# Kernel tuning notes

Hardware: AMD Instinct MI355X
Metric: run time of the kernel (lower is better)

The kernel has to match this reference:

```python
import jax, jax.numpy as jnp
import numpy as np

NEG_BIG = -1e12
ALPHA = 0.2  # LeakyReLU negative slope

def setup_inputs() -> dict:
    key = jax.random.key(0)
    k1, k2, k3, k4, k5 = jax.random.split(key, 5)
    N, F_in, F_out = 8192, 256, 128
    inp = jax.random.normal(k1, (N, F_in), dtype=jnp.float32)
    adj = jax.random.randint(k2, (N, N), 0, 2, dtype=jnp.int32)
    W = jax.random.normal(k3, (F_in, F_out), dtype=jnp.float32) * 0.05
    W_2 = jax.random.normal(k4, (F_in, F_out), dtype=jnp.float32) * 0.05
    W_3 = jax.random.normal(k5, (F_in, F_out), dtype=jnp.float32) * 0.05
    return {"inp": inp, "adj": adj, "W": W, "W_2": W_2, "W_3": W_3}

def reference(inp, adj, W, W_2, W_3):
    # h = inp @ W, h_2 = inp @ W_2  -> scores e = LeakyReLU(h @ h_2^T)  [N, N]
    h = inp @ W
    h_2 = inp @ W_2
    e = jax.nn.leaky_relu(h @ h_2.T, negative_slope=ALPHA)
    # adjacency mask, row softmax (dropout disabled: eval mode)
    attention = jax.nn.softmax(jnp.where(adj > 0, e, NEG_BIG), axis=1)
    h_3 = inp @ W_3
    h_prime = attention @ h_3
    return jax.nn.elu(h_prime)  # concat=True path
```

## Files before the change

kernel.cpp:

```cpp
#include <hip/hip_runtime.h>
#include <hip/hip_fp16.h>

#define N    8192
#define FIN  256
#define FOUT 128
#define BN   64

typedef _Float16 half8 __attribute__((ext_vector_type(8)));
typedef _Float16 half4v __attribute__((ext_vector_type(4)));
typedef float floatx4 __attribute__((ext_vector_type(4)));

__device__ __forceinline__ float exp2_fast(float x) { return __builtin_amdgcn_exp2f(x); }

__device__ __forceinline__ void gload_lds16(const void* g, void* l) {
    __builtin_amdgcn_global_load_lds(
        (const __attribute__((address_space(1))) void*)g,
        (__attribute__((address_space(3))) void*)l, 16, 0, 0);
}

__global__ __launch_bounds__(256)
void wprep_kernel(const float* __restrict__ W0,
                  const float* __restrict__ W1,
                  const float* __restrict__ W2,
                  _Float16* __restrict__ Wf)
{
    int idx  = blockIdx.x * 256 + threadIdx.x;
    int lane = idx & 63;
    int frag = idx >> 6;
    int w    = frag >> 6;
    int f    = frag & 63;
    int nt   = f >> 3, kc = f & 7;
    int quad = lane >> 4, lo16 = lane & 15;
    const float* Wp = w == 0 ? W0 : (w == 1 ? W1 : W2);
    half8 v;
#pragma unroll
    for (int jj = 0; jj < 8; jj++)
        v[jj] = (_Float16)Wp[(size_t)(kc * 32 + quad * 8 + jj) * FOUT + nt * 16 + lo16];
    *(half8*)&Wf[(size_t)idx * 8] = v;
}

__global__ __launch_bounds__(256, 2)
void gemm3_kernel(const float* __restrict__ inp,
                  const _Float16* __restrict__ Wf,
                  _Float16* __restrict__ H,
                  _Float16* __restrict__ H2,
                  _Float16* __restrict__ H3T)
{
    const int which = blockIdx.z;
    const int c0    = blockIdx.y * 64;
    const _Float16* Wfw = Wf + (size_t)which * 64 * 64 * 8;
    const int r0 = blockIdx.x * 64;
    const int tid  = threadIdx.x;
    const int wave = tid >> 6;
    const int lane = tid & 63;
    const int lo16 = lane & 15;
    const int quad = lane >> 4;
    const int r = r0 + wave * 16 + lo16;

    half8 a[8];
#pragma unroll
    for (int kc = 0; kc < 8; kc++) {
        const float* p = &inp[(size_t)r * FIN + kc * 32 + quad * 8];
        float4 v0 = *(const float4*)p;
        float4 v1 = *(const float4*)(p + 4);
        a[kc][0] = (_Float16)v0.x; a[kc][1] = (_Float16)v0.y;
        a[kc][2] = (_Float16)v0.z; a[kc][3] = (_Float16)v0.w;
        a[kc][4] = (_Float16)v1.x; a[kc][5] = (_Float16)v1.y;
        a[kc][6] = (_Float16)v1.z; a[kc][7] = (_Float16)v1.w;
    }

    floatx4 acc[4];
#pragma unroll
    for (int i = 0; i < 4; i++) acc[i] = (floatx4){0.f, 0.f, 0.f, 0.f};

#pragma unroll
    for (int kc = 0; kc < 8; kc++)
#pragma unroll
        for (int nt = 0; nt < 4; nt++) {
            int ntg = (c0 >> 4) + nt;
            half8 b = *(const half8*)&Wfw[(((size_t)ntg * 8 + kc) * 64 + lane) * 8];
            acc[nt] = __builtin_amdgcn_mfma_f32_16x16x32_f16(a[kc], b, acc[nt], 0, 0, 0);
        }

    const int arow = wave * 16 + quad * 4;
    if (which < 2) {
        _Float16* outp = which == 0 ? H : H2;
        const float scale = which == 0 ? 1.44269504f : 1.0f;
#pragma unroll
        for (int nt = 0; nt < 4; nt++)
#pragma unroll
            for (int rr = 0; rr < 4; rr++)
                outp[(size_t)(r0 + arow + rr) * FOUT + c0 + nt * 16 + lo16] =
                    (_Float16)(acc[nt][rr] * scale);
    } else {
#pragma unroll
        for (int nt = 0; nt < 4; nt++) {
            half4v v;
#pragma unroll
            for (int rr = 0; rr < 4; rr++) v[rr] = (_Float16)acc[nt][rr];
            *(half4v*)&H3T[(size_t)(c0 + nt * 16 + lo16) * N + r0 + arow] = v;
        }
    }
}

__global__ __launch_bounds__(256)
void repackKV_kernel(const _Float16* __restrict__ H2,
                     const _Float16* __restrict__ H3T,
                     _Float16* __restrict__ Kf,
                     _Float16* __restrict__ Vf)
{
    if (blockIdx.x < 512) {
        int idx  = blockIdx.x * 256 + threadIdx.x;
        int lane = idx & 63;
        int frag = idx >> 6;
        int jb = frag >> 4, f = frag & 15;
        int c = f >> 3, ntj = (f >> 2) & 1, kc = f & 3;
        int quad = lane >> 4, lo16 = lane & 15;
        int srcrow = jb * 64 + c * 32 + (lo16 >> 2) * 8 + ntj * 4 + (lo16 & 3);
        half8 v = *(const half8*)&H2[(size_t)srcrow * FOUT + kc * 32 + quad * 8];
        *(half8*)&Kf[(size_t)idx * 8] = v;
    } else {
        int idx  = (blockIdx.x - 512) * 256 + threadIdx.x;
        int lane = idx & 63;
        int frag = idx >> 6;
        int jb = frag >> 4, f = frag & 15, nt = f >> 1, kc = f & 1;
        int quad = lane >> 4, lo16 = lane & 15;
        half8 v = *(const half8*)&H3T[(size_t)(nt * 16 + lo16) * N + jb * 64 + kc * 32 + quad * 8];
        *(half8*)&Vf[(size_t)idx * 8] = v;
    }
}

template<int JS>
__global__ __launch_bounds__(256, 2)
void attn_kernel(const _Float16* __restrict__ Hq,
                 const _Float16* __restrict__ Kf,
                 const _Float16* __restrict__ Vf,
                 const int* __restrict__ adj,
                 float* __restrict__ OpartT,
                 float* __restrict__ mpart,
                 float* __restrict__ lpart)
{
    __shared__ __align__(16) _Float16 KV[2][16384];

    const int tid  = threadIdx.x;
    const int wave = tid >> 6;
    const int lane = tid & 63;
    const int lo16 = lane & 15;
    const int quad = lane >> 4;
    const int bid  = blockIdx.x;
    const int js   = bid & (JS - 1);
    const int ib   = bid / JS;
    const int iw   = ib * 128 + wave * 32;
    const int jbeg = js * (N / JS);
    const int NIT  = (N / JS) / BN;
    const int jb0  = jbeg >> 6;

    half8 q[2][4];
#pragma unroll
    for (int isub = 0; isub < 2; isub++)
#pragma unroll
        for (int kc = 0; kc < 4; kc++)
            q[isub][kc] = *(const half8*)&Hq[(size_t)(iw + isub * 16 + lo16) * FOUT + kc * 32 + quad * 8];

    floatx4 O[8][2];
#pragma unroll
    for (int nt = 0; nt < 8; nt++)
#pragma unroll
        for (int s = 0; s < 2; s++) O[nt][s] = (floatx4){0.f, 0.f, 0.f, 0.f};
    float m_s[2] = {-1e12f, -1e12f}, l_s[2] = {0.f, 0.f};

    const int* abase0 = adj + (size_t)(iw + lo16) * N + jbeg + quad * 8;
    const int* abase1 = abase0 + (size_t)16 * N;

    int4 avA[8], avB[8];

    auto LOADAV = [&](int4 (&av)[8], int it) {
        const int* b0 = abase0 + it * BN;
        const int* b1 = abase1 + it * BN;
        av[0] = *(const int4*)(b0 + 0);
        av[1] = *(const int4*)(b0 + 4);
        av[2] = *(const int4*)(b0 + 32);
        av[3] = *(const int4*)(b0 + 36);
        av[4] = *(const int4*)(b1 + 0);
        av[5] = *(const int4*)(b1 + 4);
        av[6] = *(const int4*)(b1 + 32);
        av[7] = *(const int4*)(b1 + 36);
    };

    auto STAGE = [&](int nxt, int jbn) {
        const _Float16* gk = Kf + (size_t)jbn * 8192;
        const _Float16* gv = Vf + (size_t)jbn * 8192;
#pragma unroll
        for (int r = 0; r < 4; r++) {
            int goff = (r * 256 + tid) * 8;
            int loff = (r * 256 + wave * 64) * 8;
            gload_lds16(gk + goff, &KV[nxt][loff]);
            gload_lds16(gv + goff, &KV[nxt][8192 + loff]);
        }
    };

    STAGE(0, jb0);
    LOADAV(avA, 0);
    __syncthreads();

    auto ITER = [&](int it, int4 (&avc)[8], int4 (&avn)[8], int cur) {
        if (it + 1 < NIT) {
            STAGE(cur ^ 1, jb0 + it + 1);
            LOADAV(avn, it + 1);
        }

        const _Float16* kb = &KV[cur][0];
        const _Float16* vb = &KV[cur][8192];

        floatx4 S[2][2][2];
#pragma unroll
        for (int c = 0; c < 2; c++)
#pragma unroll
            for (int ntj = 0; ntj < 2; ntj++) {
                S[c][ntj][0] = (floatx4){0.f, 0.f, 0.f, 0.f};
                S[c][ntj][1] = (floatx4){0.f, 0.f, 0.f, 0.f};
#pragma unroll
                for (int kc = 0; kc < 4; kc++) {
                    half8 kf = *(const half8*)&kb[(((c * 2 + ntj) * 4 + kc) * 64 + lane) * 8];
                    S[c][ntj][0] = __builtin_amdgcn_mfma_f32_16x16x32_f16(kf, q[0][kc], S[c][ntj][0], 0, 0, 0);
                    S[c][ntj][1] = __builtin_amdgcn_mfma_f32_16x16x32_f16(kf, q[1][kc], S[c][ntj][1], 0, 0, 0);
                }
            }

        half8 pb[2][2];
#pragma unroll
        for (int s = 0; s < 2; s++) {
            float mx = -1e12f;
#pragma unroll
            for (int c = 0; c < 2; c++)
#pragma unroll
                for (int ntj = 0; ntj < 2; ntj++)
#pragma unroll
                    for (int r = 0; r < 4; r++) {
                        float e = S[c][ntj][s][r];
                        e = fmaxf(e, 0.2f * e);
                        S[c][ntj][s][r] = e;
                        mx = fmaxf(mx, e);
                    }
            mx = fmaxf(mx, __shfl_xor(mx, 16));
            mx = fmaxf(mx, __shfl_xor(mx, 32));
            if (__any(mx > m_s[s] + 5.75f)) {
                float mn = fmaxf(m_s[s], mx);
                float al = exp2_fast(m_s[s] - mn);
                m_s[s] = mn;
                l_s[s] *= al;
#pragma unroll
                for (int nt = 0; nt < 8; nt++)
#pragma unroll
                    for (int r = 0; r < 4; r++)
                        O[nt][s][r] *= al;
            }

            float sum = 0.f;
#pragma unroll
            for (int c = 0; c < 2; c++)
#pragma unroll
                for (int ntj = 0; ntj < 2; ntj++) {
                    int4 av = avc[s * 4 + c * 2 + ntj];
#pragma unroll
                    for (int r = 0; r < 4; r++) {
                        float e = S[c][ntj][s][r] - m_s[s];
                        int a = (r == 0) ? av.x : (r == 1) ? av.y : (r == 2) ? av.z : av.w;
                        float p = (a != 0) ? exp2_fast(e) : 0.f;
                        sum += p;
                        pb[s][c][ntj * 4 + r] = (_Float16)p;
                    }
                }
            sum += __shfl_xor(sum, 16);
            sum += __shfl_xor(sum, 32);
            l_s[s] += sum;
        }

#pragma unroll
        for (int c = 0; c < 2; c++)
#pragma unroll
            for (int nt = 0; nt < 8; nt++) {
                half8 vf = *(const half8*)&vb[((nt * 2 + c) * 64 + lane) * 8];
                O[nt][0] = __builtin_amdgcn_mfma_f32_16x16x32_f16(vf, pb[0][c], O[nt][0], 0, 0, 0);
                O[nt][1] = __builtin_amdgcn_mfma_f32_16x16x32_f16(vf, pb[1][c], O[nt][1], 0, 0, 0);
            }

        __syncthreads();
    };

    for (int it2 = 0; it2 < NIT; it2 += 2) {
        ITER(it2,     avA, avB, 0);
        ITER(it2 + 1, avB, avA, 1);
    }

#pragma unroll
    for (int nt = 0; nt < 8; nt++)
#pragma unroll
        for (int s = 0; s < 2; s++)
#pragma unroll
            for (int r = 0; r < 4; r++) {
                int f = nt * 16 + quad * 4 + r;
                int i = iw + s * 16 + lo16;
                OpartT[((size_t)js * FOUT + f) * N + i] = O[nt][s][r];
            }
    if (quad == 0) {
#pragma unroll
        for (int s = 0; s < 2; s++) {
            mpart[js * N + iw + s * 16 + lo16] = m_s[s];
            lpart[js * N + iw + s * 16 + lo16] = l_s[s];
        }
    }
}

template<int JS>
__global__ __launch_bounds__(256)
void combine_kernel(const float* __restrict__ OpartT,
                    const float* __restrict__ mpart,
                    const float* __restrict__ lpart,
                    float* __restrict__ out)
{
    int idx = blockIdx.x * 256 + threadIdx.x;
    int f  = idx >> 11;
    int i4 = (idx & 2047) << 2;

    float4 M = {-3e38f, -3e38f, -3e38f, -3e38f};
    float4 m[JS];
#pragma unroll
    for (int s = 0; s < JS; s++) {
        m[s] = *(const float4*)&mpart[s * N + i4];
        M.x = fmaxf(M.x, m[s].x); M.y = fmaxf(M.y, m[s].y);
        M.z = fmaxf(M.z, m[s].z); M.w = fmaxf(M.w, m[s].w);
    }
    float4 L = {0.f, 0.f, 0.f, 0.f};
    float4 o = {0.f, 0.f, 0.f, 0.f};
#pragma unroll
    for (int s = 0; s < JS; s++) {
        float4 l = *(const float4*)&lpart[s * N + i4];
        float4 w;
        w.x = exp2_fast(m[s].x - M.x); w.y = exp2_fast(m[s].y - M.y);
        w.z = exp2_fast(m[s].z - M.z); w.w = exp2_fast(m[s].w - M.w);
        L.x += l.x * w.x; L.y += l.y * w.y;
        L.z += l.z * w.z; L.w += l.w * w.w;
        float4 v = *(const float4*)&OpartT[((size_t)s * FOUT + f) * N + i4];
        o.x += w.x * v.x; o.y += w.y * v.y;
        o.z += w.z * v.z; o.w += w.w * v.w;
    }
    float r0 = o.x / L.x, r1 = o.y / L.y, r2 = o.z / L.z, r3 = o.w / L.w;
    out[(size_t)(i4 + 0) * FOUT + f] = r0 > 0.f ? r0 : __expf(r0) - 1.f;
    out[(size_t)(i4 + 1) * FOUT + f] = r1 > 0.f ? r1 : __expf(r1) - 1.f;
    out[(size_t)(i4 + 2) * FOUT + f] = r2 > 0.f ? r2 : __expf(r2) - 1.f;
    out[(size_t)(i4 + 3) * FOUT + f] = r3 > 0.f ? r3 : __expf(r3) - 1.f;
}

extern "C" void kernel_launch(void* const* d_in, const int* in_sizes, int n_in,
                              void* d_out, int out_size, void* d_ws, size_t ws_size,
                              hipStream_t stream) {
    const float* inp = (const float*)d_in[0];
    const int*   adj = (const int*)d_in[1];
    const float* W0  = (const float*)d_in[2];
    const float* W1  = (const float*)d_in[3];
    const float* W2  = (const float*)d_in[4];
    float* out = (float*)d_out;

    constexpr int JS = 8;
    char* ws = (char*)d_ws;
    _Float16* H    = (_Float16*)(ws);
    _Float16* H2   = (_Float16*)(ws + (2u << 20));
    _Float16* H3T  = (_Float16*)(ws + (4u << 20));
    _Float16* Wf   = (_Float16*)(ws + (6u << 20));
    _Float16* Kf   = (_Float16*)(ws + (7u << 20));
    _Float16* Vf   = (_Float16*)(ws + (9u << 20));
    float* OpartT  = (float*)(ws + (11u << 20));
    float* mpart   = (float*)(ws + (43u << 20));
    float* lpart   = (float*)(ws + (43u << 20) + (size_t)JS * N * sizeof(float));

    wprep_kernel<<<48, 256, 0, stream>>>(W0, W1, W2, Wf);
    gemm3_kernel<<<dim3(N / 64, 2, 3), 256, 0, stream>>>(inp, Wf, H, H2, H3T);
    repackKV_kernel<<<1024, 256, 0, stream>>>(H2, H3T, Kf, Vf);
    attn_kernel<JS><<<(N / 128) * JS, 256, 0, stream>>>(H, Kf, Vf, adj, OpartT, mpart, lpart);
    combine_kernel<JS><<<(FOUT * (N / 4)) / 256, 256, 0, stream>>>(OpartT, mpart, lpart, out);
}
```

Before: 425.3 us.

## Split attention block into 8 waves of 16 rows and bit-pack adjacency mask

The attention kernel now launches 512 threads per block, and each wave handles 16 query rows instead of 32. Per-wave register state (Q fragments, O accumulators, adjacency prefetch) is halved, which should raise occupancy and latency hiding. The adjacency prefetch is converted into a 16-bit mask at the start of each iteration instead of keeping two full int4 buffers. In exchange, each K/V fragment read from LDS is used by one MFMA instead of two, so LDS traffic per unit of compute doubles. Barrier cost is also shared across more waves.

Result: no change. 423.5 us (-0.4%).

```diff
diff --git a/kernel.cpp b/kernel.cpp
--- a/kernel.cpp
+++ b/kernel.cpp
@@ -131,7 +131,7 @@
 }
 
 template<int JS>
-__global__ __launch_bounds__(256, 2)
+__global__ __launch_bounds__(512, 2)
 void attn_kernel(const _Float16* __restrict__ Hq,
                  const _Float16* __restrict__ Kf,
                  const _Float16* __restrict__ Vf,
@@ -150,165 +150,154 @@
     const int bid  = blockIdx.x;
     const int js   = bid & (JS - 1);
     const int ib   = bid / JS;
-    const int iw   = ib * 128 + wave * 32;
+    const int iw   = ib * 128 + wave * 16;
+    const int irow = iw + lo16;
     const int jbeg = js * (N / JS);
     const int NIT  = (N / JS) / BN;
     const int jb0  = jbeg >> 6;
 
-    half8 q[2][4];
-#pragma unroll
-    for (int isub = 0; isub < 2; isub++)
-#pragma unroll
-        for (int kc = 0; kc < 4; kc++)
-            q[isub][kc] = *(const half8*)&Hq[(size_t)(iw + isub * 16 + lo16) * FOUT + kc * 32 + quad * 8];
-
-    floatx4 O[8][2];
-#pragma unroll
-    for (int nt = 0; nt < 8; nt++)
-#pragma unroll
-        for (int s = 0; s < 2; s++) O[nt][s] = (floatx4){0.f, 0.f, 0.f, 0.f};
-    float m_s[2] = {-1e12f, -1e12f}, l_s[2] = {0.f, 0.f};
-
-    const int* abase0 = adj + (size_t)(iw + lo16) * N + jbeg + quad * 8;
-    const int* abase1 = abase0 + (size_t)16 * N;
-
-    int4 avA[8], avB[8];
-
-    auto LOADAV = [&](int4 (&av)[8], int it) {
-        const int* b0 = abase0 + it * BN;
-        const int* b1 = abase1 + it * BN;
-        av[0] = *(const int4*)(b0 + 0);
-        av[1] = *(const int4*)(b0 + 4);
-        av[2] = *(const int4*)(b0 + 32);
-        av[3] = *(const int4*)(b0 + 36);
-        av[4] = *(const int4*)(b1 + 0);
-        av[5] = *(const int4*)(b1 + 4);
-        av[6] = *(const int4*)(b1 + 32);
-        av[7] = *(const int4*)(b1 + 36);
+    half8 q[4];
+#pragma unroll
+    for (int kc = 0; kc < 4; kc++)
+        q[kc] = *(const half8*)&Hq[(size_t)irow * FOUT + kc * 32 + quad * 8];
+
+    floatx4 O[8];
+#pragma unroll
+    for (int nt = 0; nt < 8; nt++) O[nt] = (floatx4){0.f, 0.f, 0.f, 0.f};
+    float m_s = -1e12f, l_s = 0.f;
+
+    const int* abase = adj + (size_t)irow * N + jbeg + quad * 8;
+
+    int4 pv[4];
+    auto LOADAV = [&](int it) {
+        const int* b = abase + it * BN;
+        pv[0] = *(const int4*)(b + 0);
+        pv[1] = *(const int4*)(b + 4);
+        pv[2] = *(const int4*)(b + 32);
+        pv[3] = *(const int4*)(b + 36);
+    };
+    auto PACK = [&]() -> unsigned {
+        unsigned m = 0;
+        m |= (pv[0].x != 0) ? 1u << 0  : 0u;  m |= (pv[0].y != 0) ? 1u << 1  : 0u;
+        m |= (pv[0].z != 0) ? 1u << 2  : 0u;  m |= (pv[0].w != 0) ? 1u << 3  : 0u;
+        m |= (pv[1].x != 0) ? 1u << 4  : 0u;  m |= (pv[1].y != 0) ? 1u << 5  : 0u;
+        m |= (pv[1].z != 0) ? 1u << 6  : 0u;  m |= (pv[1].w != 0) ? 1u << 7  : 0u;
+        m |= (pv[2].x != 0) ? 1u << 8  : 0u;  m |= (pv[2].y != 0) ? 1u << 9  : 0u;
+        m |= (pv[2].z != 0) ? 1u << 10 : 0u;  m |= (pv[2].w != 0) ? 1u << 11 : 0u;
+        m |= (pv[3].x != 0) ? 1u << 12 : 0u;  m |= (pv[3].y != 0) ? 1u << 13 : 0u;
+        m |= (pv[3].z != 0) ? 1u << 14 : 0u;  m |= (pv[3].w != 0) ? 1u << 15 : 0u;
+        return m;
     };
 
     auto STAGE = [&](int nxt, int jbn) {
         const _Float16* gk = Kf + (size_t)jbn * 8192;
         const _Float16* gv = Vf + (size_t)jbn * 8192;
 #pragma unroll
-        for (int r = 0; r < 4; r++) {
-            int goff = (r * 256 + tid) * 8;
-            int loff = (r * 256 + wave * 64) * 8;
+        for (int r = 0; r < 2; r++) {
+            int goff = (r * 512 + tid) * 8;
+            int loff = (r * 512 + wave * 64) * 8;
             gload_lds16(gk + goff, &KV[nxt][loff]);
             gload_lds16(gv + goff, &KV[nxt][8192 + loff]);
         }
     };
 
     STAGE(0, jb0);
-    LOADAV(avA, 0);
+    LOADAV(0);
     __syncthreads();
 
-    auto ITER = [&](int it, int4 (&avc)[8], int4 (&avn)[8], int cur) {
+    auto ITER = [&](int it, int cur) {
+        unsigned mcur = PACK();
         if (it + 1 < NIT) {
             STAGE(cur ^ 1, jb0 + it + 1);
-            LOADAV(avn, it + 1);
+            LOADAV(it + 1);
         }
 
         const _Float16* kb = &KV[cur][0];
         const _Float16* vb = &KV[cur][8192];
 
-        floatx4 S[2][2][2];
+        floatx4 S[2][2];
 #pragma unroll
         for (int c = 0; c < 2; c++)
 #pragma unroll
             for (int ntj = 0; ntj < 2; ntj++) {
-                S[c][ntj][0] = (floatx4){0.f, 0.f, 0.f, 0.f};
-                S[c][ntj][1] = (floatx4){0.f, 0.f, 0.f, 0.f};
+                S[c][ntj] = (floatx4){0.f, 0.f, 0.f, 0.f};
 #pragma unroll
                 for (int kc = 0; kc < 4; kc++) {
                     half8 kf = *(const half8*)&kb[(((c * 2 + ntj) * 4 + kc) * 64 + lane) * 8];
-                    S[c][ntj][0] = __builtin_amdgcn_mfma_f32_16x16x32_f16(kf, q[0][kc], S[c][ntj][0], 0, 0, 0);
-                    S[c][ntj][1] = __builtin_amdgcn_mfma_f32_16x16x32_f16(kf, q[1][kc], S[c][ntj][1], 0, 0, 0);
+                    S[c][ntj] = __builtin_amdgcn_mfma_f32_16x16x32_f16(kf, q[kc], S[c][ntj], 0, 0, 0);
                 }
             }
 
-        half8 pb[2][2];
-#pragma unroll
-        for (int s = 0; s < 2; s++) {
-            float mx = -1e12f;
-#pragma unroll
-            for (int c = 0; c < 2; c++)
-#pragma unroll
-                for (int ntj = 0; ntj < 2; ntj++)
-#pragma unroll
-                    for (int r = 0; r < 4; r++) {
-                        float e = S[c][ntj][s][r];
-                        e = fmaxf(e, 0.2f * e);
-                        S[c][ntj][s][r] = e;
-                        mx = fmaxf(mx, e);
-                    }
-            mx = fmaxf(mx, __shfl_xor(mx, 16));
-            mx = fmaxf(mx, __shfl_xor(mx, 32));
-            if (__any(mx > m_s[s] + 5.75f)) {
-                float mn = fmaxf(m_s[s], mx);
-                float al = exp2_fast(m_s[s] - mn);
-                m_s[s] = mn;
-                l_s[s] *= al;
-#pragma unroll
-                for (int nt = 0; nt < 8; nt++)
-#pragma unroll
-                    for (int r = 0; r < 4; r++)
-                        O[nt][s][r] *= al;
-            }
-
-            float sum = 0.f;
-#pragma unroll
-            for (int c = 0; c < 2; c++)
-#pragma unroll
-                for (int ntj = 0; ntj < 2; ntj++) {
-                    int4 av = avc[s * 4 + c * 2 + ntj];
-#pragma unroll
-                    for (int r = 0; r < 4; r++) {
-                        float e = S[c][ntj][s][r] - m_s[s];
-                        int a = (r == 0) ? av.x : (r == 1) ? av.y : (r == 2) ? av.z : av.w;
-                        float p = (a != 0) ? exp2_fast(e) : 0.f;
-                        sum += p;
-                        pb[s][c][ntj * 4 + r] = (_Float16)p;
-                    }
+        float mx = -1e12f;
+#pragma unroll
+        for (int c = 0; c < 2; c++)
+#pragma unroll
+            for (int ntj = 0; ntj < 2; ntj++)
+#pragma unroll
+                for (int r = 0; r < 4; r++) {
+                    float e = S[c][ntj][r];
+                    e = fmaxf(e, 0.2f * e);
+                    S[c][ntj][r] = e;
+                    mx = fmaxf(mx, e);
                 }
-            sum += __shfl_xor(sum, 16);
-            sum += __shfl_xor(sum, 32);
-            l_s[s] += sum;
-        }
+        mx = fmaxf(mx, __shfl_xor(mx, 16));
+        mx = fmaxf(mx, __shfl_xor(mx, 32));
+        if (__any(mx > m_s + 5.75f)) {
+            float mn = fmaxf(m_s, mx);
+            float al = exp2_fast(m_s - mn);
+            m_s = mn;
+            l_s *= al;
+#pragma unroll
+            for (int nt = 0; nt < 8; nt++)
+#pragma unroll
+                for (int r = 0; r < 4; r++)
+                    O[nt][r] *= al;
+        }
+
+        half8 pb[2];
+        float sum = 0.f;
+#pragma unroll
+        for (int c = 0; c < 2; c++)
+#pragma unroll
+            for (int ntj = 0; ntj < 2; ntj++)
+#pragma unroll
+                for (int r = 0; r < 4; r++) {
+                    float e = S[c][ntj][r] - m_s;
+                    bool bit = (mcur >> (c * 8 + ntj * 4 + r)) & 1u;
+                    float p = bit ? exp2_fast(e) : 0.f;
+                    sum += p;
+                    pb[c][ntj * 4 + r] = (_Float16)p;
+                }
+        sum += __shfl_xor(sum, 16);
+        sum += __shfl_xor(sum, 32);
+        l_s += sum;
 
 #pragma unroll
         for (int c = 0; c < 2; c++)
 #pragma unroll
             for (int nt = 0; nt < 8; nt++) {
                 half8 vf = *(const half8*)&vb[((nt * 2 + c) * 64 + lane) * 8];
-                O[nt][0] = __builtin_amdgcn_mfma_f32_16x16x32_f16(vf, pb[0][c], O[nt][0], 0, 0, 0);
-                O[nt][1] = __builtin_amdgcn_mfma_f32_16x16x32_f16(vf, pb[1][c], O[nt][1], 0, 0, 0);
+                O[nt] = __builtin_amdgcn_mfma_f32_16x16x32_f16(vf, pb[c], O[nt], 0, 0, 0);
             }
 
         __syncthreads();
     };
 
     for (int it2 = 0; it2 < NIT; it2 += 2) {
-        ITER(it2,     avA, avB, 0);
-        ITER(it2 + 1, avB, avA, 1);
+        ITER(it2,     0);
+        ITER(it2 + 1, 1);
     }
 
 #pragma unroll
     for (int nt = 0; nt < 8; nt++)
 #pragma unroll
-        for (int s = 0; s < 2; s++)
-#pragma unroll
-            for (int r = 0; r < 4; r++) {
-                int f = nt * 16 + quad * 4 + r;
-                int i = iw + s * 16 + lo16;
-                OpartT[((size_t)js * FOUT + f) * N + i] = O[nt][s][r];
-            }
+        for (int r = 0; r < 4; r++) {
+            int f = nt * 16 + quad * 4 + r;
+            OpartT[((size_t)js * FOUT + f) * N + irow] = O[nt][r];
+        }
     if (quad == 0) {
-#pragma unroll
-        for (int s = 0; s < 2; s++) {
-            mpart[js * N + iw + s * 16 + lo16] = m_s[s];
-            lpart[js * N + iw + s * 16 + lo16] = l_s[s];
-        }
+        mpart[js * N + irow] = m_s;
+        lpart[js * N + irow] = l_s;
     }
 }
 
@@ -377,6 +366,6 @@
     wprep_kernel<<<48, 256, 0, stream>>>(W0, W1, W2, Wf);
     gemm3_kernel<<<dim3(N / 64, 2, 3), 256, 0, stream>>>(inp, Wf, H, H2, H3T);
     repackKV_kernel<<<1024, 256, 0, stream>>>(H2, H3T, Kf, Vf);
-    attn_kernel<JS><<<(N / 128) * JS, 256, 0, stream>>>(H, Kf, Vf, adj, OpartT, mpart, lpart);
+    attn_kernel<JS><<<(N / 128) * JS, 512, 0, stream>>>(H, Kf, Vf, adj, OpartT, mpart, lpart);
     combine_kernel<JS><<<(FOUT * (N / 4)) / 256, 256, 0, stream>>>(OpartT, mpart, lpart, out);
 }
```
